# Kernel tuning notes

Hardware: AMD Instinct MI355X
Metric: run time of the kernel (lower is better)

Reference implementation:

```python
import jax, jax.numpy as jnp
import numpy as np

D = 256      # d_model
NH = 8       # heads
NL = 3       # layers
DFF = 1024   # ffn hidden
WIN = 64     # attention window
EPS = 1e-5


def _sin_pos_embed(L, d):
    # Sinusoidal positional embedding, matches _create_pos_embedding.
    pos = jnp.arange(L, dtype=jnp.float32)[:, None]
    div = jnp.exp(jnp.arange(0, d, 2, dtype=jnp.float32) * (-np.log(10000.0) / d))
    pe = jnp.zeros((L, d), jnp.float32)
    pe = pe.at[:, 0::2].set(jnp.sin(pos * div))
    pe = pe.at[:, 1::2].set(jnp.cos(pos * div))
    return pe  # [L, D]


def _layer_norm(x, scale, bias):
    m = jnp.mean(x, axis=-1, keepdims=True)
    v = jnp.mean(jnp.square(x - m), axis=-1, keepdims=True)
    return (x - m) * jax.lax.rsqrt(v + EPS) * scale + bias


def _mha(x, Wi, bi, Wo, bo):
    # x: [N, S, D]; Wi: [3D, D]; Wo: [D, D]. torch nn.MultiheadAttention semantics (eval, no dropout).
    N, S, _ = x.shape
    dh = D // NH
    qkv = x @ Wi.T + bi                       # [N, S, 3D]
    q, k, v = jnp.split(qkv, 3, axis=-1)
    q = q.reshape(N, S, NH, dh).transpose(0, 2, 1, 3) * (dh ** -0.5)
    k = k.reshape(N, S, NH, dh).transpose(0, 2, 1, 3)
    v = v.reshape(N, S, NH, dh).transpose(0, 2, 1, 3)
    attn = jax.nn.softmax(jnp.einsum('nhqd,nhkd->nhqk', q, k), axis=-1)
    out = jnp.einsum('nhqk,nhkd->nhqd', attn, v)
    out = out.transpose(0, 2, 1, 3).reshape(N, S, D)
    return out @ Wo.T + bo


def setup_inputs() -> dict:
    key = jax.random.key(0)
    ks = jax.random.split(key, 16)
    s = 0.02
    return {
        'features': jax.random.normal(ks[0], (32, D, 32, 32), jnp.float32),
        'in_proj_w': jax.random.normal(ks[1], (NL, 3 * D, D), jnp.float32) * s,
        'in_proj_b': jnp.zeros((NL, 3 * D), jnp.float32),
        'out_proj_w': jax.random.normal(ks[2], (NL, D, D), jnp.float32) * s,
        'out_proj_b': jnp.zeros((NL, D), jnp.float32),
        'w1': jax.random.normal(ks[3], (NL, DFF, D), jnp.float32) * s,
        'b1': jnp.zeros((NL, DFF), jnp.float32),
        'w2': jax.random.normal(ks[4], (NL, D, DFF), jnp.float32) * s,
        'b2': jnp.zeros((NL, D), jnp.float32),
        'ln1_s': jnp.ones((NL, D), jnp.float32),
        'ln1_b': jnp.zeros((NL, D), jnp.float32),
        'ln2_s': jnp.ones((NL, D), jnp.float32),
        'ln2_b': jnp.zeros((NL, D), jnp.float32),
        'fnorm_s': jnp.ones((D,), jnp.float32),
        'fnorm_b': jnp.zeros((D,), jnp.float32),
    }


def reference(features, in_proj_w, in_proj_b, out_proj_w, out_proj_b,
              w1, b1, w2, b2, ln1_s, ln1_b, ln2_s, ln2_b, fnorm_s, fnorm_b):
    B, C, H, W = features.shape
    L = H * W
    x = features.reshape(B, C, L).transpose(0, 2, 1)   # [B, L, D]
    x = x + _sin_pos_embed(L, D)[None]                 # L == 1024 == max_len, no interp
    nw = L // WIN                                      # non-overlapping windows
    for i in range(NL):
        # windowed self-attention: all windows batched in one MHA call
        xw = x.reshape(B * nw, WIN, D)
        att = _mha(xw, in_proj_w[i], in_proj_b[i], out_proj_w[i], out_proj_b[i])
        att = att.reshape(B, L, D)
        x = _layer_norm(x + att, ln1_s[i], ln1_b[i])
        h = jax.nn.gelu(x @ w1[i].T + b1[i], approximate=False) @ w2[i].T + b2[i]
        x = _layer_norm(x + h, ln2_s[i], ln2_b[i])
    x = _layer_norm(x, fnorm_s, fnorm_b)
    return x.transpose(0, 2, 1).reshape(B, C, H, W)
```

## Files before the change

kernel.cpp:

```cpp
#include <hip/hip_runtime.h>
#include <hip/hip_bf16.h>

#define BSZ 32
#define DM 256
#define LSEQ 1024
#define MTOK (BSZ * LSEQ)
#define NHEAD 8
#define DHEAD 32
#define WIN 64
#define DFF 1024
#define M8 ((size_t)MTOK * 8)

typedef short bf16x8 __attribute__((ext_vector_type(8)));
typedef float f32x4 __attribute__((ext_vector_type(4)));
typedef unsigned short u16x8 __attribute__((ext_vector_type(8)));

union BF { __hip_bfloat16 h; unsigned short u; };
__device__ __forceinline__ unsigned short f2bf(float f) { BF b; b.h = __float2bfloat16(f); return b.u; }
__device__ __forceinline__ float bf2f(unsigned short u) { return __uint_as_float((unsigned)u << 16); }

#define GLD_LDS16(gp, lp) __builtin_amdgcn_global_load_lds( \
    (const __attribute__((address_space(1))) void*)(gp),    \
    (__attribute__((address_space(3))) void*)(lp), 16, 0, 0)

__device__ __forceinline__ float gelu_fast(float x) {
    float t = x * (0.7978845608f + 0.0356774081f * x * x);
    return x / (1.0f + __expf(-2.0f * t));
}

__global__ __launch_bounds__(256) void cvt_kernel(
    const float* __restrict__ s, unsigned short* __restrict__ d,
    int N, int K, int nl)
{
    int K8 = K >> 3;
    int per = N * K8;
    int c = blockIdx.x * 256 + threadIdx.x;
    if (c >= per * nl) return;
    int layer = c / per, rem = c - layer * per;
    int n = rem / K8, kc = rem - n * K8;
    const float* sp = s + (size_t)layer * N * K + (size_t)n * K + kc * 8;
    float4 v0 = *(const float4*)sp, v1 = *(const float4*)(sp + 4);
    uint4 o;
    o.x = f2bf(v0.x) | ((unsigned)f2bf(v0.y) << 16);
    o.y = f2bf(v0.z) | ((unsigned)f2bf(v0.w) << 16);
    o.z = f2bf(v1.x) | ((unsigned)f2bf(v1.y) << 16);
    o.w = f2bf(v1.z) | ((unsigned)f2bf(v1.w) << 16);
    *(uint4*)(d + (size_t)layer * N * K + (size_t)kc * N * 8 + (size_t)n * 8) = o;
}

__global__ __launch_bounds__(256) void pe_kernel(float* __restrict__ PE)
{
    int l = blockIdx.x, c = threadIdx.x;
    int i2 = c & ~1;
    float div = expf(-9.210340371976184f * (float)i2 / 256.0f);
    float ang = (float)l * div;
    PE[l * DM + c] = (c & 1) ? cosf(ang) : sinf(ang);
}

__global__ __launch_bounds__(256) void embed_kernel(
    const float* __restrict__ F, const float* __restrict__ PE,
    float* __restrict__ Xf, unsigned short* __restrict__ Xb)
{
    __shared__ float tile[64][65];
    int b = blockIdx.z, l0 = blockIdx.y * 64, c0 = blockIdx.x * 64;
    int tid = threadIdx.x;
    int li = tid & 63, c4 = tid >> 6;
    #pragma unroll
    for (int it = 0; it < 16; ++it) {
        int c = c4 + it * 4;
        tile[c][li] = F[((size_t)(b * DM + c0 + c)) * LSEQ + l0 + li];
    }
    __syncthreads();
    int ci = tid & 63, l4 = tid >> 6;
    #pragma unroll
    for (int it = 0; it < 16; ++it) {
        int l = l4 + it * 4;
        float x = tile[ci][l] + PE[(l0 + l) * DM + c0 + ci];
        Xf[((size_t)b * LSEQ + l0 + l) * DM + c0 + ci] = x;
    }
    int ch = tid >> 5;
    int lx = tid & 31;
    #pragma unroll
    for (int rd = 0; rd < 2; ++rd) {
        int l = lx + rd * 32;
        unsigned short vs[8];
        #pragma unroll
        for (int e = 0; e < 8; ++e) {
            int c = ch * 8 + e;
            vs[e] = f2bf(tile[c][l] + PE[(l0 + l) * DM + c0 + c]);
        }
        uint4 o;
        o.x = vs[0] | ((unsigned)vs[1] << 16);
        o.y = vs[2] | ((unsigned)vs[3] << 16);
        o.z = vs[4] | ((unsigned)vs[5] << 16);
        o.w = vs[6] | ((unsigned)vs[7] << 16);
        *(uint4*)(Xb + ((size_t)((c0 >> 3) + ch)) * M8 +
                  (size_t)(b * LSEQ + l0 + l) * 8) = o;
    }
}

__global__ __launch_bounds__(256) void gemm_mfma_kernel(
    const unsigned short* __restrict__ A, const unsigned short* __restrict__ Bw,
    const float* __restrict__ bias, unsigned short* __restrict__ Cb,
    int M, int N, int K, int gelu)
{
    const int tid = threadIdx.x;
    const int lane = tid & 63, wave = tid >> 6;
    const int l15 = lane & 15, quad = lane >> 4;
    const int wm = (wave & 1) * 64, wn = (wave >> 1) * 64;
    const int m0 = blockIdx.x * 128, n0 = blockIdx.y * 128;
    const size_t Ma8 = (size_t)M * 8, Nb8 = (size_t)N * 8;
    const size_t astep = 4 * Ma8, bstep = 4 * Nb8;

    const unsigned short* ap[4];
    const unsigned short* bp[4];
    #pragma unroll
    for (int i = 0; i < 4; ++i)
        ap[i] = A + quad * Ma8 + (size_t)(m0 + wm + i * 16 + l15) * 8;
    #pragma unroll
    for (int j = 0; j < 4; ++j)
        bp[j] = Bw + quad * Nb8 + (size_t)(n0 + wn + j * 16 + l15) * 8;

    f32x4 acc[4][4] = {};
    bf16x8 aA[4], bA[4], aB[4], bB[4];
    #pragma unroll
    for (int i = 0; i < 4; ++i) aA[i] = *(const bf16x8*)(ap[i]);
    #pragma unroll
    for (int j = 0; j < 4; ++j) bA[j] = *(const bf16x8*)(bp[j]);

    const int iters = K >> 5;
    for (int t = 0; t < iters; t += 2) {
        size_t o1 = (size_t)(t + 1);
        #pragma unroll
        for (int i = 0; i < 4; ++i) aB[i] = *(const bf16x8*)(ap[i] + o1 * astep);
        #pragma unroll
        for (int j = 0; j < 4; ++j) bB[j] = *(const bf16x8*)(bp[j] + o1 * bstep);
        #pragma unroll
        for (int i = 0; i < 4; ++i)
            #pragma unroll
            for (int j = 0; j < 4; ++j)
                acc[i][j] = __builtin_amdgcn_mfma_f32_16x16x32_bf16(
                    bA[j], aA[i], acc[i][j], 0, 0, 0);
        size_t o2 = (size_t)((t + 2 < iters) ? t + 2 : iters - 1);
        #pragma unroll
        for (int i = 0; i < 4; ++i) aA[i] = *(const bf16x8*)(ap[i] + o2 * astep);
        #pragma unroll
        for (int j = 0; j < 4; ++j) bA[j] = *(const bf16x8*)(bp[j] + o2 * bstep);
        #pragma unroll
        for (int i = 0; i < 4; ++i)
            #pragma unroll
            for (int j = 0; j < 4; ++j)
                acc[i][j] = __builtin_amdgcn_mfma_f32_16x16x32_bf16(
                    bB[j], aB[i], acc[i][j], 0, 0, 0);
    }

    float4 bb[4];
    #pragma unroll
    for (int j = 0; j < 4; ++j)
        bb[j] = *(const float4*)(bias + n0 + wn + j * 16 + quad * 4);

    #pragma unroll
    for (int i = 0; i < 4; ++i) {
        const size_t m8 = (size_t)(m0 + wm + i * 16 + l15) * 8;
        #pragma unroll
        for (int j = 0; j < 4; ++j) {
            int nb = n0 + wn + j * 16 + quad * 4;
            float v0 = acc[i][j][0] + bb[j].x;
            float v1 = acc[i][j][1] + bb[j].y;
            float v2 = acc[i][j][2] + bb[j].z;
            float v3 = acc[i][j][3] + bb[j].w;
            if (gelu) {
                v0 = gelu_fast(v0); v1 = gelu_fast(v1);
                v2 = gelu_fast(v2); v3 = gelu_fast(v3);
            }
            uint2 o;
            o.x = f2bf(v0) | ((unsigned)f2bf(v1) << 16);
            o.y = f2bf(v2) | ((unsigned)f2bf(v3) << 16);
            *(uint2*)(Cb + ((size_t)(nb >> 3)) * Ma8 + m8 + (nb & 7)) = o;
        }
    }
}

__global__ __launch_bounds__(256) void gemm_ln_kernel(
    const unsigned short* __restrict__ A, const unsigned short* __restrict__ Bw,
    const float* __restrict__ bias, const float* __restrict__ resid,
    const float* __restrict__ lns, const float* __restrict__ lnb,
    float* __restrict__ Xf, unsigned short* __restrict__ Xb, int K)
{
    __shared__ float Ss[256], Sq[256];
    const int tid = threadIdx.x;
    const int lane = tid & 63, wave = tid >> 6;
    const int l15 = lane & 15, quad = lane >> 4;
    const int wn = wave * 64;
    const int m0 = blockIdx.x * 64;
    const size_t Nb8 = (size_t)DM * 8;
    const size_t astep = 4 * M8, bstep = 4 * Nb8;

    const unsigned short* ap[4];
    const unsigned short* bp[4];
    #pragma unroll
    for (int i = 0; i < 4; ++i)
        ap[i] = A + quad * M8 + (size_t)(m0 + i * 16 + l15) * 8;
    #pragma unroll
    for (int j = 0; j < 4; ++j)
        bp[j] = Bw + quad * Nb8 + (size_t)(wn + j * 16 + l15) * 8;

    f32x4 acc[4][4] = {};
    bf16x8 aA[4], bA[4], aB[4], bB[4];
    #pragma unroll
    for (int i = 0; i < 4; ++i) aA[i] = *(const bf16x8*)(ap[i]);
    #pragma unroll
    for (int j = 0; j < 4; ++j) bA[j] = *(const bf16x8*)(bp[j]);

    const int iters = K >> 5;
    for (int t = 0; t < iters; t += 2) {
        size_t o1 = (size_t)(t + 1);
        #pragma unroll
        for (int i = 0; i < 4; ++i) aB[i] = *(const bf16x8*)(ap[i] + o1 * astep);
        #pragma unroll
        for (int j = 0; j < 4; ++j) bB[j] = *(const bf16x8*)(bp[j] + o1 * bstep);
        #pragma unroll
        for (int i = 0; i < 4; ++i)
            #pragma unroll
            for (int j = 0; j < 4; ++j)
                acc[i][j] = __builtin_amdgcn_mfma_f32_16x16x32_bf16(
                    bA[j], aA[i], acc[i][j], 0, 0, 0);
        size_t o2 = (size_t)((t + 2 < iters) ? t + 2 : iters - 1);
        #pragma unroll
        for (int i = 0; i < 4; ++i) aA[i] = *(const bf16x8*)(ap[i] + o2 * astep);
        #pragma unroll
        for (int j = 0; j < 4; ++j) bA[j] = *(const bf16x8*)(bp[j] + o2 * bstep);
        #pragma unroll
        for (int i = 0; i < 4; ++i)
            #pragma unroll
            for (int j = 0; j < 4; ++j)
                acc[i][j] = __builtin_amdgcn_mfma_f32_16x16x32_bf16(
                    bB[j], aB[i], acc[i][j], 0, 0, 0);
    }

    float4 bj[4];
    #pragma unroll
    for (int j = 0; j < 4; ++j)
        bj[j] = *(const float4*)(bias + wn + j * 16 + quad * 4);
    #pragma unroll
    for (int i = 0; i < 4; ++i) {
        const float* rp = resid + (size_t)(m0 + i * 16 + l15) * DM + wn + quad * 4;
        #pragma unroll
        for (int j = 0; j < 4; ++j) {
            float4 rr = *(const float4*)(rp + j * 16);
            acc[i][j][0] += bj[j].x + rr.x;
            acc[i][j][1] += bj[j].y + rr.y;
            acc[i][j][2] += bj[j].z + rr.z;
            acc[i][j][3] += bj[j].w + rr.w;
        }
    }

    #pragma unroll
    for (int i = 0; i < 4; ++i) {
        float s = 0.f, q = 0.f;
        #pragma unroll
        for (int j = 0; j < 4; ++j)
            #pragma unroll
            for (int r = 0; r < 4; ++r) {
                float x = acc[i][j][r];
                s += x; q = fmaf(x, x, q);
            }
        s += __shfl_xor(s, 16); q += __shfl_xor(q, 16);
        s += __shfl_xor(s, 32); q += __shfl_xor(q, 32);
        if (quad == 0) {
            Ss[wave * 64 + i * 16 + l15] = s;
            Sq[wave * 64 + i * 16 + l15] = q;
        }
    }
    __syncthreads();

    float4 scj[4], bbj[4];
    #pragma unroll
    for (int j = 0; j < 4; ++j) {
        scj[j] = *(const float4*)(lns + wn + j * 16 + quad * 4);
        bbj[j] = *(const float4*)(lnb + wn + j * 16 + quad * 4);
    }
    #pragma unroll
    for (int i = 0; i < 4; ++i) {
        int row = i * 16 + l15;
        float s = Ss[row] + Ss[64 + row] + Ss[128 + row] + Ss[192 + row];
        float q = Sq[row] + Sq[64 + row] + Sq[128 + row] + Sq[192 + row];
        float mean = s * (1.0f / 256.0f);
        float var  = q * (1.0f / 256.0f) - mean * mean;
        float rinv = rsqrtf(var + 1e-5f);
        #pragma unroll
        for (int j = 0; j < 4; ++j) {
            acc[i][j][0] = (acc[i][j][0] - mean) * rinv * scj[j].x + bbj[j].x;
            acc[i][j][1] = (acc[i][j][1] - mean) * rinv * scj[j].y + bbj[j].y;
            acc[i][j][2] = (acc[i][j][2] - mean) * rinv * scj[j].z + bbj[j].z;
            acc[i][j][3] = (acc[i][j][3] - mean) * rinv * scj[j].w + bbj[j].w;
        }
    }

    #pragma unroll
    for (int i = 0; i < 4; ++i) {
        int m = m0 + i * 16 + l15;
        size_t gf = (size_t)m * DM + wn + quad * 4;
        size_t m8 = (size_t)m * 8;
        #pragma unroll
        for (int j = 0; j < 4; ++j) {
            float4 o = { acc[i][j][0], acc[i][j][1], acc[i][j][2], acc[i][j][3] };
            *(float4*)(Xf + gf + j * 16) = o;
            int nb = wn + j * 16 + quad * 4;
            uint2 ob;
            ob.x = f2bf(o.x) | ((unsigned)f2bf(o.y) << 16);
            ob.y = f2bf(o.z) | ((unsigned)f2bf(o.w) << 16);
            *(uint2*)(Xb + ((size_t)(nb >> 3)) * M8 + m8 + (nb & 7)) = ob;
        }
    }
}

__global__ __launch_bounds__(64) void attn_mfma_kernel(
    const unsigned short* __restrict__ QKV, unsigned short* __restrict__ ATT)
{
    __shared__ __align__(16) char smem[22016];
    unsigned short* Qs = (unsigned short*)smem;
    unsigned short* Ks = (unsigned short*)(smem + 4096);
    unsigned short* VT = (unsigned short*)(smem + 8192);
    unsigned short* Ps = (unsigned short*)(smem + 12800);
    float*          Po = (float*)(smem + 12800);

    const int wg = blockIdx.x, h = blockIdx.y;
    const int base = wg * WIN;
    const int lane = threadIdx.x;
    const int l15 = lane & 15, quad = lane >> 4;
    const float scale = 0.17677669529663687f;

    #pragma unroll
    for (int dc = 0; dc < 4; ++dc) {
        GLD_LDS16(QKV + ((size_t)(h * 4 + dc)) * M8 + (size_t)(base + lane) * 8,
                  Qs + dc * 512 + (size_t)lane * 8);
        GLD_LDS16(QKV + ((size_t)(32 + h * 4 + dc)) * M8 + (size_t)(base + lane) * 8,
                  Ks + dc * 512 + (size_t)lane * 8);
    }
    u16x8 vv[4];
    #pragma unroll
    for (int cc = 0; cc < 4; ++cc)
        vv[cc] = *(const u16x8*)(QKV + ((size_t)(64 + h * 4 + cc)) * M8 +
                                 (size_t)(base + lane) * 8);
    #pragma unroll
    for (int cc = 0; cc < 4; ++cc)
        #pragma unroll
        for (int e = 0; e < 8; ++e)
            VT[(cc * 8 + e) * 72 + lane] = vv[cc][e];
    __syncthreads();

    const f32x4 zero4 = {0.f, 0.f, 0.f, 0.f};
    bf16x8 aq[4], bk[4];
    #pragma unroll
    for (int i = 0; i < 4; ++i)
        aq[i] = *(const bf16x8*)(Qs + quad * 512 + (i * 16 + l15) * 8);
    #pragma unroll
    for (int j = 0; j < 4; ++j)
        bk[j] = *(const bf16x8*)(Ks + quad * 512 + (j * 16 + l15) * 8);
    f32x4 S[4][4];
    #pragma unroll
    for (int i = 0; i < 4; ++i)
        #pragma unroll
        for (int j = 0; j < 4; ++j)
            S[i][j] = __builtin_amdgcn_mfma_f32_16x16x32_bf16(aq[i], bk[j], zero4, 0, 0, 0);

    float mx[4][4], sum[4][4];
    #pragma unroll
    for (int i = 0; i < 4; ++i)
        #pragma unroll
        for (int r = 0; r < 4; ++r) {
            float m0 = -1e30f;
            #pragma unroll
            for (int j = 0; j < 4; ++j) {
                S[i][j][r] *= scale;
                m0 = fmaxf(m0, S[i][j][r]);
            }
            mx[i][r] = m0;
        }
    #pragma unroll
    for (int off = 1; off < 16; off <<= 1)
        #pragma unroll
        for (int i = 0; i < 4; ++i)
            #pragma unroll
            for (int r = 0; r < 4; ++r)
                mx[i][r] = fmaxf(mx[i][r], __shfl_xor(mx[i][r], off));
    #pragma unroll
    for (int i = 0; i < 4; ++i)
        #pragma unroll
        for (int r = 0; r < 4; ++r) {
            float s0 = 0.f;
            #pragma unroll
            for (int j = 0; j < 4; ++j) {
                float e = __expf(S[i][j][r] - mx[i][r]);
                S[i][j][r] = e;
                s0 += e;
            }
            sum[i][r] = s0;
        }
    #pragma unroll
    for (int off = 1; off < 16; off <<= 1)
        #pragma unroll
        for (int i = 0; i < 4; ++i)
            #pragma unroll
            for (int r = 0; r < 4; ++r)
                sum[i][r] += __shfl_xor(sum[i][r], off);

    #pragma unroll
    for (int i = 0; i < 4; ++i)
        #pragma unroll
        for (int r = 0; r < 4; ++r) {
            float inv = 1.0f / sum[i][r];
            #pragma unroll
            for (int j = 0; j < 4; ++j)
                Ps[(i * 16 + quad * 4 + r) * 72 + j * 16 + l15] =
                    f2bf(S[i][j][r] * inv);
        }
    asm volatile("s_waitcnt lgkmcnt(0)" ::: "memory");

    bf16x8 ap0[4], ap1[4], bv0[2], bv1[2];
    #pragma unroll
    for (int i = 0; i < 4; ++i) {
        ap0[i] = *(const bf16x8*)(Ps + (i * 16 + l15) * 72 + quad * 8);
        ap1[i] = *(const bf16x8*)(Ps + (i * 16 + l15) * 72 + 32 + quad * 8);
    }
    #pragma unroll
    for (int jd = 0; jd < 2; ++jd) {
        bv0[jd] = *(const bf16x8*)(VT + (jd * 16 + l15) * 72 + quad * 8);
        bv1[jd] = *(const bf16x8*)(VT + (jd * 16 + l15) * 72 + 32 + quad * 8);
    }
    f32x4 O[4][2];
    #pragma unroll
    for (int i = 0; i < 4; ++i)
        #pragma unroll
        for (int jd = 0; jd < 2; ++jd) {
            f32x4 t = __builtin_amdgcn_mfma_f32_16x16x32_bf16(ap0[i], bv0[jd], zero4, 0, 0, 0);
            O[i][jd] = __builtin_amdgcn_mfma_f32_16x16x32_bf16(ap1[i], bv1[jd], t, 0, 0, 0);
        }
    asm volatile("s_waitcnt lgkmcnt(0)" ::: "memory");

    #pragma unroll
    for (int i = 0; i < 4; ++i)
        #pragma unroll
        for (int jd = 0; jd < 2; ++jd)
            #pragma unroll
            for (int r = 0; r < 4; ++r)
                Po[(i * 16 + quad * 4 + r) * 36 + jd * 16 + l15] = O[i][jd][r];
    asm volatile("s_waitcnt lgkmcnt(0)" ::: "memory");

    #pragma unroll
    for (int g = 0; g < 4; ++g) {
        f32x4 t0 = *(const f32x4*)(Po + lane * 36 + g * 8);
        f32x4 t1 = *(const f32x4*)(Po + lane * 36 + g * 8 + 4);
        uint4 w;
        w.x = f2bf(t0[0]) | ((unsigned)f2bf(t0[1]) << 16);
        w.y = f2bf(t0[2]) | ((unsigned)f2bf(t0[3]) << 16);
        w.z = f2bf(t1[0]) | ((unsigned)f2bf(t1[1]) << 16);
        w.w = f2bf(t1[2]) | ((unsigned)f2bf(t1[3]) << 16);
        *(uint4*)(ATT + ((size_t)(h * 4 + g)) * M8 + (size_t)(base + lane) * 8) = w;
    }
}

__global__ __launch_bounds__(256) void out_ln_kernel(
    const float* __restrict__ Xf, const float* __restrict__ sc,
    const float* __restrict__ bi, float* __restrict__ out)
{
    __shared__ float tile[64][257];
    __shared__ float mean_s[64], rinv_s[64];
    int b = blockIdx.y, l0 = blockIdx.x * 64;
    int tid = threadIdx.x, wave = tid >> 6, lane = tid & 63;
    int c = lane * 4;
    #pragma unroll
    for (int it = 0; it < 16; ++it) {
        int tl = wave * 16 + it;
        float4 v = *(const float4*)(Xf + ((size_t)(b * LSEQ + l0 + tl)) * DM + c);
        *(float4*)&tile[tl][c] = v;
        float sm = v.x + v.y + v.z + v.w;
        float sq = v.x * v.x + v.y * v.y + v.z * v.z + v.w * v.w;
        #pragma unroll
        for (int off = 32; off > 0; off >>= 1) {
            sm += __shfl_down(sm, off);
            sq += __shfl_down(sq, off);
        }
        if (lane == 0) {
            float mean = sm * (1.0f / 256.0f);
            float var  = sq * (1.0f / 256.0f) - mean * mean;
            mean_s[tl] = mean;
            rinv_s[tl] = rsqrtf(var + 1e-5f);
        }
    }
    __syncthreads();
    int lout = tid & 63, crow = tid >> 6;
    #pragma unroll
    for (int ct = 0; ct < 4; ++ct) {
        int c0 = ct * 64;
        #pragma unroll
        for (int it = 0; it < 16; ++it) {
            int cc = c0 + crow + it * 4;
            float v = tile[lout][cc];
            out[((size_t)(b * DM + cc)) * LSEQ + l0 + lout] =
                (v - mean_s[lout]) * rinv_s[lout] * sc[cc] + bi[cc];
        }
    }
}

extern "C" void kernel_launch(void* const* d_in, const int* in_sizes, int n_in,
                              void* d_out, int out_size, void* d_ws, size_t ws_size,
                              hipStream_t stream)
{
    const float* F   = (const float*)d_in[0];
    const float* Wi  = (const float*)d_in[1];
    const float* Bi  = (const float*)d_in[2];
    const float* Wo  = (const float*)d_in[3];
    const float* Bo  = (const float*)d_in[4];
    const float* W1  = (const float*)d_in[5];
    const float* B1  = (const float*)d_in[6];
    const float* W2  = (const float*)d_in[7];
    const float* B2  = (const float*)d_in[8];
    const float* L1s = (const float*)d_in[9];
    const float* L1b = (const float*)d_in[10];
    const float* L2s = (const float*)d_in[11];
    const float* L2b = (const float*)d_in[12];
    const float* Fs  = (const float*)d_in[13];
    const float* Fb  = (const float*)d_in[14];

    char* w = (char*)d_ws;
    float*          Xf   = (float*)w;
    unsigned short* QKVb = (unsigned short*)(w + 33554432);
    unsigned short* Hb   = (unsigned short*)(w + 83886080);
    unsigned short* Xb   = (unsigned short*)(w + 150994944);
    unsigned short* ATTb = (unsigned short*)(w + 167772160);
    unsigned short* WB   = (unsigned short*)(w + 184549376);
    float*          PE   = (float*)(w + 189267968);
    unsigned short* Wib  = WB;
    unsigned short* Wob  = WB + 589824;
    unsigned short* W1b  = WB + 786432;
    unsigned short* W2b  = WB + 1572864;

    cvt_kernel<<<(3 * 768 * 32 + 255) / 256, 256, 0, stream>>>(Wi, Wib, 768, 256, 3);
    cvt_kernel<<<(3 * 256 * 32 + 255) / 256, 256, 0, stream>>>(Wo, Wob, 256, 256, 3);
    cvt_kernel<<<(3 * 1024 * 32 + 255) / 256, 256, 0, stream>>>(W1, W1b, 1024, 256, 3);
    cvt_kernel<<<(3 * 256 * 128 + 255) / 256, 256, 0, stream>>>(W2, W2b, 256, 1024, 3);
    pe_kernel<<<LSEQ, 256, 0, stream>>>(PE);
    embed_kernel<<<dim3(DM / 64, LSEQ / 64, BSZ), 256, 0, stream>>>(F, PE, Xf, Xb);

    for (int i = 0; i < 3; ++i) {
        gemm_mfma_kernel<<<dim3(MTOK / 128, 768 / 128), 256, 0, stream>>>(
            Xb, Wib + (size_t)i * 196608, Bi + i * 768, QKVb, MTOK, 768, DM, 0);
        attn_mfma_kernel<<<dim3(BSZ * (LSEQ / WIN), NHEAD), 64, 0, stream>>>(QKVb, ATTb);
        gemm_ln_kernel<<<MTOK / 64, 256, 0, stream>>>(
            ATTb, Wob + (size_t)i * 65536, Bo + i * DM, Xf,
            L1s + i * DM, L1b + i * DM, Xf, Xb, DM);
        gemm_mfma_kernel<<<dim3(MTOK / 128, DFF / 128), 256, 0, stream>>>(
            Xb, W1b + (size_t)i * 262144, B1 + i * DFF, Hb, MTOK, DFF, DM, 1);
        gemm_ln_kernel<<<MTOK / 64, 256, 0, stream>>>(
            Hb, W2b + (size_t)i * 262144, B2 + i * DM, Xf,
            L2s + i * DM, L2b + i * DM, Xf, Xb, DFF);
    }

    out_ln_kernel<<<dim3(LSEQ / 64, BSZ), 256, 0, stream>>>(
        Xf, Fs, Fb, (float*)d_out);
}
```

Baseline: 579.2 us.

## Fuse FFN up-projection, GELU, down-projection and LayerNorm into one kernel

Replaces the separate W1 GEMM+GELU kernel and W2 GEMM+LayerNorm kernel with a single kernel per 64-token block. The kernel walks the 1024-wide hidden dimension in four 256-wide chunks, keeps each GELU output chunk in LDS as bf16, and accumulates the W2 product in registers. The intent is to avoid writing and re-reading the 32K x 1024 bf16 hidden activation through global memory and to drop one launch per layer. In exchange, the W1 and W2 operands are loaded straight from global memory with no LDS staging, register pressure is high (two 4x4 accumulator sets), and there are only 512 blocks with added barriers, which may lower occupancy and MFMA utilisation.

```diff
diff --git a/kernel.cpp b/kernel.cpp
--- a/kernel.cpp
+++ b/kernel.cpp
@@ -305,6 +305,212 @@
         #pragma unroll
         for (int j = 0; j < 4; ++j) {
             float4 o = { acc[i][j][0], acc[i][j][1], acc[i][j][2], acc[i][j][3] };
+            *(float4*)(Xf + gf + j * 16) = o;
+            int nb = wn + j * 16 + quad * 4;
+            uint2 ob;
+            ob.x = f2bf(o.x) | ((unsigned)f2bf(o.y) << 16);
+            ob.y = f2bf(o.z) | ((unsigned)f2bf(o.w) << 16);
+            *(uint2*)(Xb + ((size_t)(nb >> 3)) * M8 + m8 + (nb & 7)) = ob;
+        }
+    }
+}
+
+__global__ __launch_bounds__(256, 2) void ffn_fused_kernel(
+    const unsigned short* __restrict__ A, const unsigned short* __restrict__ W1w,
+    const float* __restrict__ b1, const unsigned short* __restrict__ W2w,
+    const float* __restrict__ b2, const float* __restrict__ resid,
+    const float* __restrict__ lns, const float* __restrict__ lnb,
+    float* __restrict__ Xf, unsigned short* __restrict__ Xb)
+{
+    __shared__ unsigned short Hlds[16384];
+    __shared__ float Ss[256], Sq[256];
+    const int tid = threadIdx.x;
+    const int lane = tid & 63, wave = tid >> 6;
+    const int l15 = lane & 15, quad = lane >> 4;
+    const int wn = wave * 64;
+    const int m0 = blockIdx.x * 64;
+    const size_t N1b8 = (size_t)DFF * 8;
+    const size_t astep = 4 * M8, b1step = 4 * N1b8;
+
+    const unsigned short* ap[4];
+    #pragma unroll
+    for (int i = 0; i < 4; ++i)
+        ap[i] = A + quad * M8 + (size_t)(m0 + i * 16 + l15) * 8;
+
+    f32x4 acc2[4][4] = {};
+
+    for (int qq = 0; qq < 4; ++qq) {
+        const unsigned short* bp[4];
+        #pragma unroll
+        for (int j = 0; j < 4; ++j)
+            bp[j] = W1w + quad * N1b8 + (size_t)(qq * 256 + wn + j * 16 + l15) * 8;
+
+        f32x4 acc1[4][4] = {};
+        {
+            bf16x8 aA[4], bA[4], aB[4], bB[4];
+            #pragma unroll
+            for (int i = 0; i < 4; ++i) aA[i] = *(const bf16x8*)(ap[i]);
+            #pragma unroll
+            for (int j = 0; j < 4; ++j) bA[j] = *(const bf16x8*)(bp[j]);
+            for (int t = 0; t < 8; t += 2) {
+                size_t o1 = (size_t)(t + 1);
+                #pragma unroll
+                for (int i = 0; i < 4; ++i) aB[i] = *(const bf16x8*)(ap[i] + o1 * astep);
+                #pragma unroll
+                for (int j = 0; j < 4; ++j) bB[j] = *(const bf16x8*)(bp[j] + o1 * b1step);
+                #pragma unroll
+                for (int i = 0; i < 4; ++i)
+                    #pragma unroll
+                    for (int j = 0; j < 4; ++j)
+                        acc1[i][j] = __builtin_amdgcn_mfma_f32_16x16x32_bf16(
+                            bA[j], aA[i], acc1[i][j], 0, 0, 0);
+                size_t o2 = (size_t)((t + 2 < 8) ? t + 2 : 7);
+                #pragma unroll
+                for (int i = 0; i < 4; ++i) aA[i] = *(const bf16x8*)(ap[i] + o2 * astep);
+                #pragma unroll
+                for (int j = 0; j < 4; ++j) bA[j] = *(const bf16x8*)(bp[j] + o2 * b1step);
+                #pragma unroll
+                for (int i = 0; i < 4; ++i)
+                    #pragma unroll
+                    for (int j = 0; j < 4; ++j)
+                        acc1[i][j] = __builtin_amdgcn_mfma_f32_16x16x32_bf16(
+                            bB[j], aB[i], acc1[i][j], 0, 0, 0);
+            }
+        }
+        {
+            float4 bb[4];
+            #pragma unroll
+            for (int j = 0; j < 4; ++j)
+                bb[j] = *(const float4*)(b1 + qq * 256 + wn + j * 16 + quad * 4);
+            #pragma unroll
+            for (int i = 0; i < 4; ++i) {
+                int m = i * 16 + l15;
+                #pragma unroll
+                for (int j = 0; j < 4; ++j) {
+                    float v0 = gelu_fast(acc1[i][j][0] + bb[j].x);
+                    float v1 = gelu_fast(acc1[i][j][1] + bb[j].y);
+                    float v2 = gelu_fast(acc1[i][j][2] + bb[j].z);
+                    float v3 = gelu_fast(acc1[i][j][3] + bb[j].w);
+                    int chunk = wave * 8 + j * 2 + (quad >> 1);
+                    uint2 o;
+                    o.x = f2bf(v0) | ((unsigned)f2bf(v1) << 16);
+                    o.y = f2bf(v2) | ((unsigned)f2bf(v3) << 16);
+                    *(uint2*)(Hlds + chunk * 512 + m * 8 + (quad & 1) * 4) = o;
+                }
+            }
+        }
+        __syncthreads();
+
+        {
+            const unsigned short* b2p[4];
+            #pragma unroll
+            for (int j = 0; j < 4; ++j)
+                b2p[j] = W2w + ((size_t)(qq * 32 + quad)) * 2048 +
+                         (size_t)(wn + j * 16 + l15) * 8;
+            bf16x8 hA[4], w2A[4], w2B[4];
+            #pragma unroll
+            for (int j = 0; j < 4; ++j) w2A[j] = *(const bf16x8*)(b2p[j]);
+            for (int t = 0; t < 8; t += 2) {
+                size_t o1 = (size_t)(t + 1);
+                #pragma unroll
+                for (int j = 0; j < 4; ++j)
+                    w2B[j] = *(const bf16x8*)(b2p[j] + o1 * 8192);
+                #pragma unroll
+                for (int i = 0; i < 4; ++i)
+                    hA[i] = *(const bf16x8*)(Hlds + (t * 4 + quad) * 512 +
+                                             (i * 16 + l15) * 8);
+                #pragma unroll
+                for (int i = 0; i < 4; ++i)
+                    #pragma unroll
+                    for (int j = 0; j < 4; ++j)
+                        acc2[i][j] = __builtin_amdgcn_mfma_f32_16x16x32_bf16(
+                            w2A[j], hA[i], acc2[i][j], 0, 0, 0);
+                size_t o2 = (size_t)((t + 2 < 8) ? t + 2 : 7);
+                #pragma unroll
+                for (int j = 0; j < 4; ++j)
+                    w2A[j] = *(const bf16x8*)(b2p[j] + o2 * 8192);
+                #pragma unroll
+                for (int i = 0; i < 4; ++i)
+                    hA[i] = *(const bf16x8*)(Hlds + ((t + 1) * 4 + quad) * 512 +
+                                             (i * 16 + l15) * 8);
+                #pragma unroll
+                for (int i = 0; i < 4; ++i)
+                    #pragma unroll
+                    for (int j = 0; j < 4; ++j)
+                        acc2[i][j] = __builtin_amdgcn_mfma_f32_16x16x32_bf16(
+                            w2B[j], hA[i], acc2[i][j], 0, 0, 0);
+            }
+        }
+        __syncthreads();
+    }
+
+    float4 bj[4];
+    #pragma unroll
+    for (int j = 0; j < 4; ++j)
+        bj[j] = *(const float4*)(b2 + wn + j * 16 + quad * 4);
+    #pragma unroll
+    for (int i = 0; i < 4; ++i) {
+        const float* rp = resid + (size_t)(m0 + i * 16 + l15) * DM + wn + quad * 4;
+        #pragma unroll
+        for (int j = 0; j < 4; ++j) {
+            float4 rr = *(const float4*)(rp + j * 16);
+            acc2[i][j][0] += bj[j].x + rr.x;
+            acc2[i][j][1] += bj[j].y + rr.y;
+            acc2[i][j][2] += bj[j].z + rr.z;
+            acc2[i][j][3] += bj[j].w + rr.w;
+        }
+    }
+
+    #pragma unroll
+    for (int i = 0; i < 4; ++i) {
+        float s = 0.f, q = 0.f;
+        #pragma unroll
+        for (int j = 0; j < 4; ++j)
+            #pragma unroll
+            for (int r = 0; r < 4; ++r) {
+                float x = acc2[i][j][r];
+                s += x; q = fmaf(x, x, q);
+            }
+        s += __shfl_xor(s, 16); q += __shfl_xor(q, 16);
+        s += __shfl_xor(s, 32); q += __shfl_xor(q, 32);
+        if (quad == 0) {
+            Ss[wave * 64 + i * 16 + l15] = s;
+            Sq[wave * 64 + i * 16 + l15] = q;
+        }
+    }
+    __syncthreads();
+
+    float4 scj[4], bbj[4];
+    #pragma unroll
+    for (int j = 0; j < 4; ++j) {
+        scj[j] = *(const float4*)(lns + wn + j * 16 + quad * 4);
+        bbj[j] = *(const float4*)(lnb + wn + j * 16 + quad * 4);
+    }
+    #pragma unroll
+    for (int i = 0; i < 4; ++i) {
+        int row = i * 16 + l15;
+        float s = Ss[row] + Ss[64 + row] + Ss[128 + row] + Ss[192 + row];
+        float q = Sq[row] + Sq[64 + row] + Sq[128 + row] + Sq[192 + row];
+        float mean = s * (1.0f / 256.0f);
+        float var  = q * (1.0f / 256.0f) - mean * mean;
+        float rinv = rsqrtf(var + 1e-5f);
+        #pragma unroll
+        for (int j = 0; j < 4; ++j) {
+            acc2[i][j][0] = (acc2[i][j][0] - mean) * rinv * scj[j].x + bbj[j].x;
+            acc2[i][j][1] = (acc2[i][j][1] - mean) * rinv * scj[j].y + bbj[j].y;
+            acc2[i][j][2] = (acc2[i][j][2] - mean) * rinv * scj[j].z + bbj[j].z;
+            acc2[i][j][3] = (acc2[i][j][3] - mean) * rinv * scj[j].w + bbj[j].w;
+        }
+    }
+
+    #pragma unroll
+    for (int i = 0; i < 4; ++i) {
+        int m = m0 + i * 16 + l15;
+        size_t gf = (size_t)m * DM + wn + quad * 4;
+        size_t m8 = (size_t)m * 8;
+        #pragma unroll
+        for (int j = 0; j < 4; ++j) {
+            float4 o = { acc2[i][j][0], acc2[i][j][1], acc2[i][j][2], acc2[i][j][3] };
             *(float4*)(Xf + gf + j * 16) = o;
             int nb = wn + j * 16 + quad * 4;
             uint2 ob;
@@ -536,6 +742,7 @@
     unsigned short* Wob  = WB + 589824;
     unsigned short* W1b  = WB + 786432;
     unsigned short* W2b  = WB + 1572864;
+    (void)Hb;
 
     cvt_kernel<<<(3 * 768 * 32 + 255) / 256, 256, 0, stream>>>(Wi, Wib, 768, 256, 3);
     cvt_kernel<<<(3 * 256 * 32 + 255) / 256, 256, 0, stream>>>(Wo, Wob, 256, 256, 3);
@@ -551,11 +758,10 @@
         gemm_ln_kernel<<<MTOK / 64, 256, 0, stream>>>(
             ATTb, Wob + (size_t)i * 65536, Bo + i * DM, Xf,
             L1s + i * DM, L1b + i * DM, Xf, Xb, DM);
-        gemm_mfma_kernel<<<dim3(MTOK / 128, DFF / 128), 256, 0, stream>>>(
-            Xb, W1b + (size_t)i * 262144, B1 + i * DFF, Hb, MTOK, DFF, DM, 1);
-        gemm_ln_kernel<<<MTOK / 64, 256, 0, stream>>>(
-            Hb, W2b + (size_t)i * 262144, B2 + i * DM, Xf,
-            L2s + i * DM, L2b + i * DM, Xf, Xb, DFF);
+        ffn_fused_kernel<<<MTOK / 64, 256, 0, stream>>>(
+            Xb, W1b + (size_t)i * 262144, B1 + i * DFF,
+            W2b + (size_t)i * 262144, B2 + i * DM, Xf,
+            L2s + i * DM, L2b + i * DM, Xf, Xb);
     }
 
     out_ln_kernel<<<dim3(LSEQ / 64, BSZ), 256, 0, stream>>>(
```

Measured after the change: 646.3 us. 1.12x slower.

## Fuse QKV projection GEMM into windowed attention kernel

Applied to the files above, without the earlier changes.

The separate QKV projection GEMM is removed. Each attention workgroup (one window, one head) now computes its own Q, K and V tile with MFMA directly from the bf16 activations and the in-projection weights, writing them into LDS, so the QKV buffer never goes through global memory. The cost is lower data reuse: each 64-thread workgroup reads its operands straight from global memory without LDS tiling, and the window's activations are re-read by all 8 head workgroups. Compute per workgroup also grows, with a single wave doing the GEMM serially.

```diff
diff --git a/kernel.cpp b/kernel.cpp
--- a/kernel.cpp
+++ b/kernel.cpp
@@ -18,10 +18,6 @@
 union BF { __hip_bfloat16 h; unsigned short u; };
 __device__ __forceinline__ unsigned short f2bf(float f) { BF b; b.h = __float2bfloat16(f); return b.u; }
 __device__ __forceinline__ float bf2f(unsigned short u) { return __uint_as_float((unsigned)u << 16); }
-
-#define GLD_LDS16(gp, lp) __builtin_amdgcn_global_load_lds( \
-    (const __attribute__((address_space(1))) void*)(gp),    \
-    (__attribute__((address_space(3))) void*)(lp), 16, 0, 0)
 
 __device__ __forceinline__ float gelu_fast(float x) {
     float t = x * (0.7978845608f + 0.0356774081f * x * x);
@@ -315,8 +311,9 @@
     }
 }
 
-__global__ __launch_bounds__(64) void attn_mfma_kernel(
-    const unsigned short* __restrict__ QKV, unsigned short* __restrict__ ATT)
+__global__ __launch_bounds__(64) void attn_fused_kernel(
+    const unsigned short* __restrict__ Xq, const unsigned short* __restrict__ Wiw,
+    const float* __restrict__ bi, unsigned short* __restrict__ ATT)
 {
     __shared__ __align__(16) char smem[22016];
     unsigned short* Qs = (unsigned short*)smem;
@@ -331,24 +328,67 @@
     const int l15 = lane & 15, quad = lane >> 4;
     const float scale = 0.17677669529663687f;
 
-    #pragma unroll
-    for (int dc = 0; dc < 4; ++dc) {
-        GLD_LDS16(QKV + ((size_t)(h * 4 + dc)) * M8 + (size_t)(base + lane) * 8,
-                  Qs + dc * 512 + (size_t)lane * 8);
-        GLD_LDS16(QKV + ((size_t)(32 + h * 4 + dc)) * M8 + (size_t)(base + lane) * 8,
-                  Ks + dc * 512 + (size_t)lane * 8);
-    }
-    u16x8 vv[4];
-    #pragma unroll
-    for (int cc = 0; cc < 4; ++cc)
-        vv[cc] = *(const u16x8*)(QKV + ((size_t)(64 + h * 4 + cc)) * M8 +
-                                 (size_t)(base + lane) * 8);
-    #pragma unroll
-    for (int cc = 0; cc < 4; ++cc)
-        #pragma unroll
-        for (int e = 0; e < 8; ++e)
-            VT[(cc * 8 + e) * 72 + lane] = vv[cc][e];
-    __syncthreads();
+    const size_t Nb8 = (size_t)768 * 8;
+    const size_t astep = 4 * M8, bstep = 4 * Nb8;
+
+    const unsigned short* ap[4];
+    #pragma unroll
+    for (int i = 0; i < 4; ++i)
+        ap[i] = Xq + quad * M8 + (size_t)(base + i * 16 + l15) * 8;
+
+    #pragma unroll
+    for (int p = 0; p < 3; ++p) {
+        const int n0p = p * 256 + h * 32;
+        const unsigned short* bp0 = Wiw + quad * Nb8 + (size_t)(n0p + l15) * 8;
+        const unsigned short* bp1 = bp0 + 16 * 8;
+
+        f32x4 acc[4][2] = {};
+        #pragma unroll
+        for (int t = 0; t < 8; ++t) {
+            bf16x8 b0 = *(const bf16x8*)(bp0 + (size_t)t * bstep);
+            bf16x8 b1 = *(const bf16x8*)(bp1 + (size_t)t * bstep);
+            #pragma unroll
+            for (int i = 0; i < 4; ++i) {
+                bf16x8 a = *(const bf16x8*)(ap[i] + (size_t)t * astep);
+                acc[i][0] = __builtin_amdgcn_mfma_f32_16x16x32_bf16(b0, a, acc[i][0], 0, 0, 0);
+                acc[i][1] = __builtin_amdgcn_mfma_f32_16x16x32_bf16(b1, a, acc[i][1], 0, 0, 0);
+            }
+        }
+        float4 bj0 = *(const float4*)(bi + n0p + quad * 4);
+        float4 bj1 = *(const float4*)(bi + n0p + 16 + quad * 4);
+        #pragma unroll
+        for (int i = 0; i < 4; ++i) {
+            acc[i][0][0] += bj0.x; acc[i][0][1] += bj0.y;
+            acc[i][0][2] += bj0.z; acc[i][0][3] += bj0.w;
+            acc[i][1][0] += bj1.x; acc[i][1][1] += bj1.y;
+            acc[i][1][2] += bj1.z; acc[i][1][3] += bj1.w;
+        }
+        if (p < 2) {
+            unsigned short* D = (p == 0) ? Qs : Ks;
+            #pragma unroll
+            for (int i = 0; i < 4; ++i) {
+                int t = i * 16 + l15;
+                #pragma unroll
+                for (int j = 0; j < 2; ++j) {
+                    int chunk = j * 2 + (quad >> 1);
+                    uint2 o;
+                    o.x = f2bf(acc[i][j][0]) | ((unsigned)f2bf(acc[i][j][1]) << 16);
+                    o.y = f2bf(acc[i][j][2]) | ((unsigned)f2bf(acc[i][j][3]) << 16);
+                    *(uint2*)(D + chunk * 512 + t * 8 + (quad & 1) * 4) = o;
+                }
+            }
+        } else {
+            #pragma unroll
+            for (int i = 0; i < 4; ++i)
+                #pragma unroll
+                for (int j = 0; j < 2; ++j)
+                    #pragma unroll
+                    for (int r = 0; r < 4; ++r)
+                        VT[(j * 16 + quad * 4 + r) * 72 + i * 16 + l15] =
+                            f2bf(acc[i][j][r]);
+        }
+    }
+    asm volatile("s_waitcnt lgkmcnt(0)" ::: "memory");
 
     const f32x4 zero4 = {0.f, 0.f, 0.f, 0.f};
     bf16x8 aq[4], bk[4];
@@ -526,7 +566,6 @@
 
     char* w = (char*)d_ws;
     float*          Xf   = (float*)w;
-    unsigned short* QKVb = (unsigned short*)(w + 33554432);
     unsigned short* Hb   = (unsigned short*)(w + 83886080);
     unsigned short* Xb   = (unsigned short*)(w + 150994944);
     unsigned short* ATTb = (unsigned short*)(w + 167772160);
@@ -545,9 +584,8 @@
     embed_kernel<<<dim3(DM / 64, LSEQ / 64, BSZ), 256, 0, stream>>>(F, PE, Xf, Xb);
 
     for (int i = 0; i < 3; ++i) {
-        gemm_mfma_kernel<<<dim3(MTOK / 128, 768 / 128), 256, 0, stream>>>(
-            Xb, Wib + (size_t)i * 196608, Bi + i * 768, QKVb, MTOK, 768, DM, 0);
-        attn_mfma_kernel<<<dim3(BSZ * (LSEQ / WIN), NHEAD), 64, 0, stream>>>(QKVb, ATTb);
+        attn_fused_kernel<<<dim3(BSZ * (LSEQ / WIN), NHEAD), 64, 0, stream>>>(
+            Xb, Wib + (size_t)i * 196608, Bi + i * 768, ATTb);
         gemm_ln_kernel<<<MTOK / 64, 256, 0, stream>>>(
             ATTb, Wob + (size_t)i * 65536, Bo + i * DM, Xf,
             L1s + i * DM, L1b + i * DM, Xf, Xb, DM);
```

Measured after the change: 638.7 us. 10.3% more time.
